# Kernel tuning notes

Hardware: AMD Instinct MI355X
Metric: run time of the kernel (lower is better)

## Reference

```python
import jax, jax.numpy as jnp
import numpy as np

N_UPDATE = 3

def _lin(key, fan_in, fan_out):
    s = 1.0 / np.sqrt(fan_in)
    k1, k2 = jax.random.split(key)
    W = jax.random.uniform(k1, (fan_in, fan_out), jnp.float32, -s, s)
    b = jax.random.uniform(k2, (fan_out,), jnp.float32, -s, s)
    return W, b

def setup_inputs() -> dict:
    key = jax.random.key(0)
    ks = jax.random.split(key, 12)
    N, E, F_NODE, F_EDGE, H, L, R, T = 50000, 400000, 16, 16, 32, 64, 128, 1
    inp = {}
    inp["x"] = jax.random.normal(ks[0], (N, F_NODE), jnp.float32)
    inp["edge_index"] = jax.random.randint(ks[1], (E, 2), 0, N)  # [E,2] (src,dst)
    inp["edge_attr"] = jax.random.normal(ks[2], (E, F_EDGE), jnp.float32)
    # edge MLP: F_EDGE -> 64 -> 64 -> H*H
    inp["Wm0"], inp["bm0"] = _lin(ks[3], F_EDGE, L)
    inp["Wm1"], inp["bm1"] = _lin(ks[4], L, L)
    inp["Wm2"], inp["bm2"] = _lin(ks[5], L, H * H)
    # NNConv root weight + bias
    inp["root"], inp["bias"] = _lin(ks[6], H, H)
    # readout i-net: 2H -> R -> T ; j-net: H -> R -> T
    inp["Wi0"], inp["bi0"] = _lin(ks[7], 2 * H, R)
    inp["Wi1"], inp["bi1"] = _lin(ks[8], R, T)
    inp["Wj0"], inp["bj0"] = _lin(ks[9], H, R)
    inp["Wj1"], inp["bj1"] = _lin(ks[10], R, T)
    return inp

def reference(x, edge_index, edge_attr, Wm0, bm0, Wm1, bm1, Wm2, bm2,
              root, bias, Wi0, bi0, Wi1, bi1, Wj0, bj0, Wj1, bj1):
    N = x.shape[0]
    H = root.shape[0]
    # h_0 = [x, zeros] padded to hidden_state_size
    h0 = jnp.concatenate([x, jnp.zeros((N, H - x.shape[1]), x.dtype)], axis=1)
    # edge MLP -> per-edge weight matrices (edge_attr constant across updates)
    e = jax.nn.relu(edge_attr @ Wm0 + bm0)
    e = jax.nn.relu(e @ Wm1 + bm1)
    W = (e @ Wm2 + bm2).reshape(-1, H, H)  # [E, H, H]
    src = edge_index[:, 0]
    dst = edge_index[:, 1]
    h = h0
    for _ in range(N_UPDATE):
        msg = jnp.einsum('eh,eho->eo', h[src], W)              # gather + bmm
        agg = jax.ops.segment_sum(msg, dst, num_segments=N)    # scatter-add
        h = h @ root + bias + agg                              # NNConv root/bias
    # mpnn readout: sum_v sigmoid(i([h_T, h_0])) * j(h_T)
    gate = jax.nn.sigmoid(jax.nn.relu(jnp.concatenate([h, h0], 1) @ Wi0 + bi0) @ Wi1 + bi1)
    val = jax.nn.relu(h @ Wj0 + bj0) @ Wj1 + bj1
    return jnp.sum(gate * val, axis=0)  # [target_size]
```

## Files before the change

### kernel.cpp

```cpp
#include <hip/hip_runtime.h>
#include <stdint.h>

#define N_UPDATE 3
#define HD 32
#define FN 16

typedef unsigned short u16;
typedef __bf16 bf16x8 __attribute__((ext_vector_type(8)));
typedef float f32x4 __attribute__((ext_vector_type(4)));

__device__ __forceinline__ float bf2f(u16 u) {
  union { uint32_t i; float f; } v; v.i = ((uint32_t)u) << 16; return v.f;
}
__device__ __forceinline__ u16 f2bf(float f) {
  union { uint32_t i; float f; } v; v.f = f;
  uint32_t x = v.i;
  return (u16)((x + 0x7fffu + ((x >> 16) & 1u)) >> 16);
}

union frag16 { uint4 v; bf16x8 b; u16 s[8]; };

__global__ void k_zero_f(float* __restrict__ p, int n) {
  int i = blockIdx.x * blockDim.x + threadIdx.x;
  if (i < n) p[i] = 0.f;
}
__global__ void k_zero_i(int* __restrict__ p, int n) {
  int i = blockIdx.x * blockDim.x + threadIdx.x;
  if (i < n) p[i] = 0;
}

__global__ void k_hist(const int* __restrict__ eidx, int* __restrict__ cnt, int E) {
  int e = blockIdx.x * blockDim.x + threadIdx.x;
  if (e >= E) return;
  atomicAdd(&cnt[eidx[2 * e]], 1);
}

__global__ __launch_bounds__(1024) void k_scan(const int* __restrict__ cnt,
                                               int* __restrict__ ptr, int N) {
  __shared__ int sums[1024];
  int chunk = (N + 1023) / 1024;
  int beg = threadIdx.x * chunk;
  int end = beg + chunk; if (end > N) end = N;
  int s = 0;
  for (int i = beg; i < end; i++) s += cnt[i];
  sums[threadIdx.x] = s;
  __syncthreads();
  for (int off = 1; off < 1024; off <<= 1) {
    int v = (threadIdx.x >= off) ? sums[threadIdx.x - off] : 0;
    __syncthreads();
    sums[threadIdx.x] += v;
    __syncthreads();
  }
  int run = (threadIdx.x == 0) ? 0 : sums[threadIdx.x - 1];
  for (int i = beg; i < end; i++) { ptr[i] = run; run += cnt[i]; }
}

__global__ void k_scatter(const int* __restrict__ eidx, int* __restrict__ ptr,
                          int* __restrict__ se_src, int* __restrict__ se_dst,
                          int* __restrict__ invp, int E) {
  int e = blockIdx.x * blockDim.x + threadIdx.x;
  if (e >= E) return;
  int2 sd = ((const int2*)eidx)[e];
  int pos = atomicAdd(&ptr[sd.x], 1);
  se_src[pos] = sd.x;
  se_dst[pos] = sd.y;
  invp[e] = pos;
}

__global__ void k_prep_bf(const float* __restrict__ Wm2, uint4* __restrict__ Bf) {
  int t = blockIdx.x;
  int lane = threadIdx.x;
  int col = lane & 15;
  int hg = lane >> 4;
  int p = t >> 6;
  int t2 = t & 63;
  int j2 = t2 * 16 + col;
  int o = p * 16 + (j2 >> 6);
  int k = j2 & 63;
  frag16 f;
#pragma unroll
  for (int jj = 0; jj < 8; jj++) {
    int h = hg * 8 + jj;
    f.s[jj] = f2bf(Wm2[k * 1024 + h * 32 + o]);
  }
  Bf[t * 64 + lane] = f.v;
}

__global__ void k_init_h(const float* __restrict__ x, float* __restrict__ h, int N) {
  int idx = blockIdx.x * blockDim.x + threadIdx.x;
  if (idx >= N * HD) return;
  int n = idx >> 5, c = idx & 31;
  h[idx] = (c < FN) ? x[n * FN + c] : 0.f;
}

__global__ __launch_bounds__(256) void k_edge_mlp(
    const float* __restrict__ ea,
    const float* __restrict__ Wm0, const float* __restrict__ bm0,
    const float* __restrict__ Wm1, const float* __restrict__ bm1,
    const int* __restrict__ invp, u16* __restrict__ ee, int E) {
  int e = blockIdx.x * blockDim.x + threadIdx.x;
  if (e >= E) return;
  float a[16];
  {
    const float4* p = (const float4*)(ea + (size_t)e * 16);
    float4 v0 = p[0], v1 = p[1], v2 = p[2], v3 = p[3];
    a[0]=v0.x; a[1]=v0.y; a[2]=v0.z; a[3]=v0.w;
    a[4]=v1.x; a[5]=v1.y; a[6]=v1.z; a[7]=v1.w;
    a[8]=v2.x; a[9]=v2.y; a[10]=v2.z; a[11]=v2.w;
    a[12]=v3.x; a[13]=v3.y; a[14]=v3.z; a[15]=v3.w;
  }
  float t0[64];
#pragma unroll
  for (int j = 0; j < 64; j++) t0[j] = bm0[j];
#pragma unroll
  for (int k = 0; k < 16; k++) {
    float av = a[k];
#pragma unroll
    for (int j = 0; j < 64; j++) t0[j] = fmaf(av, Wm0[k * 64 + j], t0[j]);
  }
#pragma unroll
  for (int j = 0; j < 64; j++) t0[j] = fmaxf(t0[j], 0.f);

  u16* dst = ee + (size_t)invp[e] * 64;
#pragma unroll
  for (int half = 0; half < 2; half++) {
    float t1[32];
#pragma unroll
    for (int j = 0; j < 32; j++) t1[j] = bm1[half * 32 + j];
#pragma unroll
    for (int k = 0; k < 64; k++) {
      float tv = t0[k];
#pragma unroll
      for (int j = 0; j < 32; j++) t1[j] = fmaf(tv, Wm1[k * 64 + half * 32 + j], t1[j]);
    }
    unsigned int out[16];
#pragma unroll
    for (int j = 0; j < 16; j++) {
      u16 lo = f2bf(fmaxf(t1[2 * j], 0.f));
      u16 hi = f2bf(fmaxf(t1[2 * j + 1], 0.f));
      out[j] = (unsigned int)lo | ((unsigned int)hi << 16);
    }
    uint4* op = (uint4*)(dst + half * 32);
#pragma unroll
    for (int q = 0; q < 4; q++) {
      uint4 w; w.x = out[q*4+0]; w.y = out[q*4+1]; w.z = out[q*4+2]; w.w = out[q*4+3];
      op[q] = w;
    }
  }
}

__global__ __launch_bounds__(256) void k_gemm_G(
    const float* __restrict__ h, const uint4* __restrict__ Bf,
    u16* __restrict__ Gb, int N, int p) {
  int wave = threadIdx.x >> 6;
  int lane = threadIdx.x & 63;
  int jt = blockIdx.y * 4 + wave;
  int n0 = blockIdx.x * 16;
  int row = lane & 15;
  int kg = lane >> 4;

  int nr = n0 + row; if (nr > N - 1) nr = N - 1;
  const float* hr = h + (size_t)nr * HD + kg * 8;
  float4 f0 = *(const float4*)hr;
  float4 f1 = *(const float4*)(hr + 4);
  frag16 a;
  a.s[0] = f2bf(f0.x); a.s[1] = f2bf(f0.y); a.s[2] = f2bf(f0.z); a.s[3] = f2bf(f0.w);
  a.s[4] = f2bf(f1.x); a.s[5] = f2bf(f1.y); a.s[6] = f2bf(f1.z); a.s[7] = f2bf(f1.w);

  frag16 b; b.v = Bf[(p * 64 + jt) * 64 + lane];

  f32x4 acc = {0.f, 0.f, 0.f, 0.f};
  acc = __builtin_amdgcn_mfma_f32_16x16x32_bf16(a.b, b.b, acc, 0, 0, 0);

  int j2 = jt * 16 + row;
#pragma unroll
  for (int r = 0; r < 4; r++) {
    int n = n0 + kg * 4 + r;
    if (n < N) Gb[(size_t)n * 1024 + j2] = f2bf(acc[r]);
  }
}

__global__ __launch_bounds__(256) void k_msg(
    const u16* __restrict__ Gb, const float* __restrict__ h,
    const float* __restrict__ bm2, const u16* __restrict__ ee,
    const int* __restrict__ se_src, const int* __restrict__ se_dst,
    float* __restrict__ agg, int E, int p) {
  int t = blockIdx.x * blockDim.x + threadIdx.x;
  int e = t >> 4;
  int o_l = t & 15;
  if (e >= E) return;
  int src = se_src[e];
  int dst = se_dst[e];
  int o = p * 16 + o_l;

  float hv0 = h[(size_t)src * HD + o_l];
  float hv1 = h[(size_t)src * HD + 16 + o_l];
  float acc = 0.f;
#pragma unroll
  for (int hh = 0; hh < 16; hh++) {
    acc = fmaf(__shfl(hv0, hh, 16), bm2[hh * 32 + o], acc);
    acc = fmaf(__shfl(hv1, hh, 16), bm2[(hh + 16) * 32 + o], acc);
  }

  const uint4* ep = (const uint4*)(ee + (size_t)e * 64);
  const uint4* gp = (const uint4*)(Gb + ((size_t)src * 16 + o_l) * 64);
  frag16 eu[8], gu[8];
#pragma unroll
  for (int q = 0; q < 8; q++) { eu[q].v = ep[q]; gu[q].v = gp[q]; }
#pragma unroll
  for (int k = 0; k < 64; k++) {
    acc = fmaf(bf2f(eu[k >> 3].s[k & 7]), bf2f(gu[k >> 3].s[k & 7]), acc);
  }
  atomicAdd(&agg[(size_t)dst * HD + o], acc);
}

__global__ __launch_bounds__(256) void k_update(
    const float* __restrict__ h, float* __restrict__ agg,
    const float* __restrict__ root, const float* __restrict__ bias,
    float* __restrict__ hn, int N) {
  int t = blockIdx.x * blockDim.x + threadIdx.x;
  int n = t >> 5, o = t & 31;
  if (n >= N) return;
  float hv = h[(size_t)n * HD + o];
  float acc = bias[o] + agg[(size_t)n * HD + o];
  agg[(size_t)n * HD + o] = 0.f;
#pragma unroll
  for (int k = 0; k < 32; k++)
    acc = fmaf(__shfl(hv, k, 32), root[k * HD + o], acc);
  hn[(size_t)n * HD + o] = acc;
}

__global__ __launch_bounds__(256) void k_readout(
    const float* __restrict__ h, const float* __restrict__ x,
    const float* __restrict__ Wi0, const float* __restrict__ bi0,
    const float* __restrict__ Wi1, const float* __restrict__ bi1,
    const float* __restrict__ Wj0, const float* __restrict__ bj0,
    const float* __restrict__ Wj1, const float* __restrict__ bj1,
    float* __restrict__ partial, int N) {
  int wid = threadIdx.x >> 6;
  int lane = threadIdx.x & 63;
  int n = blockIdx.x * 4 + wid;
  __shared__ float sred[4];
  float contrib = 0.f;
  if (n < N) {
    float uv;
    if (lane < 32) uv = h[(size_t)n * HD + lane];
    else if (lane < 48) uv = x[(size_t)n * FN + lane - 32];
    else uv = 0.f;

    float g1a = bi0[lane], g1b = bi0[lane + 64];
#pragma unroll
    for (int k = 0; k < 64; k++) {
      float u = __shfl(uv, k, 64);
      g1a = fmaf(u, Wi0[k * 128 + lane], g1a);
      g1b = fmaf(u, Wi0[k * 128 + lane + 64], g1b);
    }
    g1a = fmaxf(g1a, 0.f); g1b = fmaxf(g1b, 0.f);
    float gp = g1a * Wi1[lane] + g1b * Wi1[lane + 64];

    float v1a = bj0[lane], v1b = bj0[lane + 64];
#pragma unroll
    for (int k = 0; k < 32; k++) {
      float hk = __shfl(uv, k, 64);
      v1a = fmaf(hk, Wj0[k * 128 + lane], v1a);
      v1b = fmaf(hk, Wj0[k * 128 + lane + 64], v1b);
    }
    v1a = fmaxf(v1a, 0.f); v1b = fmaxf(v1b, 0.f);
    float vp = v1a * Wj1[lane] + v1b * Wj1[lane + 64];

#pragma unroll
    for (int s = 32; s; s >>= 1) {
      gp += __shfl_xor(gp, s, 64);
      vp += __shfl_xor(vp, s, 64);
    }
    float gate = 1.f / (1.f + __expf(-(gp + bi1[0])));
    float val = vp + bj1[0];
    contrib = gate * val;
  }
  if (lane == 0) sred[wid] = contrib;
  __syncthreads();
  if (threadIdx.x == 0) partial[blockIdx.x] = sred[0] + sred[1] + sred[2] + sred[3];
}

__global__ void k_final(const float* __restrict__ partial, float* __restrict__ out, int P) {
  __shared__ float sm[256];
  float s = 0.f;
  for (int i = threadIdx.x; i < P; i += 256) s += partial[i];
  sm[threadIdx.x] = s;
  __syncthreads();
  for (int st = 128; st; st >>= 1) {
    if ((int)threadIdx.x < st) sm[threadIdx.x] += sm[threadIdx.x + st];
    __syncthreads();
  }
  if (threadIdx.x == 0) out[0] = sm[0];
}

extern "C" void kernel_launch(void* const* d_in, const int* in_sizes, int n_in,
                              void* d_out, int out_size, void* d_ws, size_t ws_size,
                              hipStream_t stream) {
  const float* x    = (const float*)d_in[0];
  const int*   eidx = (const int*)d_in[1];
  const float* ea   = (const float*)d_in[2];
  const float* Wm0  = (const float*)d_in[3];
  const float* bm0  = (const float*)d_in[4];
  const float* Wm1  = (const float*)d_in[5];
  const float* bm1  = (const float*)d_in[6];
  const float* Wm2  = (const float*)d_in[7];
  const float* bm2  = (const float*)d_in[8];
  const float* root = (const float*)d_in[9];
  const float* bias = (const float*)d_in[10];
  const float* Wi0  = (const float*)d_in[11];
  const float* bi0  = (const float*)d_in[12];
  const float* Wi1  = (const float*)d_in[13];
  const float* bi1  = (const float*)d_in[14];
  const float* Wj0  = (const float*)d_in[15];
  const float* bj0  = (const float*)d_in[16];
  const float* Wj1  = (const float*)d_in[17];
  const float* bj1  = (const float*)d_in[18];

  int N = in_sizes[0] / FN;
  int E = in_sizes[1] / 2;
  int nb = (N + 3) / 4;

  auto al = [](size_t b) { return (b + 255) & ~(size_t)255; };
  size_t need = al((size_t)N * 1024 * 2) + al((size_t)E * 64 * 2) +
                al(128 * 64 * sizeof(uint4)) + 3 * al((size_t)N * HD * 4) +
                2 * al((size_t)N * 4) + 3 * al((size_t)E * 4) + al((size_t)nb * 4);
  if (need > ws_size) return;

  char* ws = (char*)d_ws;
  size_t off = 0;
  auto alloc = [&](size_t bytes) { void* p = ws + off; off += al(bytes); return p; };
  u16*   Gb      = (u16*)alloc((size_t)N * 1024 * 2);
  u16*   ee      = (u16*)alloc((size_t)E * 64 * 2);
  uint4* Bf      = (uint4*)alloc(128 * 64 * sizeof(uint4));
  float* hA      = (float*)alloc((size_t)N * HD * 4);
  float* hB      = (float*)alloc((size_t)N * HD * 4);
  float* agg     = (float*)alloc((size_t)N * HD * 4);
  int*   cnt     = (int*)alloc((size_t)N * 4);
  int*   ptr     = (int*)alloc((size_t)N * 4);
  int*   se_src  = (int*)alloc((size_t)E * 4);
  int*   se_dst  = (int*)alloc((size_t)E * 4);
  int*   invp    = (int*)alloc((size_t)E * 4);
  float* partial = (float*)alloc((size_t)nb * 4);

  int mt = (N + 15) / 16;
  int ng = (N * HD + 255) / 256;
  int eg = (E + 255) / 256;

  hipLaunchKernelGGL(k_zero_i, dim3((N + 255) / 256), dim3(256), 0, stream, cnt, N);
  hipLaunchKernelGGL(k_hist, dim3(eg), dim3(256), 0, stream, eidx, cnt, E);
  hipLaunchKernelGGL(k_scan, dim3(1), dim3(1024), 0, stream, cnt, ptr, N);
  hipLaunchKernelGGL(k_scatter, dim3(eg), dim3(256), 0, stream, eidx, ptr, se_src, se_dst, invp, E);

  hipLaunchKernelGGL(k_prep_bf, dim3(128), dim3(64), 0, stream, Wm2, Bf);
  hipLaunchKernelGGL(k_init_h, dim3(ng), dim3(256), 0, stream, x, hA, N);
  hipLaunchKernelGGL(k_edge_mlp, dim3(eg), dim3(256), 0, stream,
                     ea, Wm0, bm0, Wm1, bm1, invp, ee, E);
  hipLaunchKernelGGL(k_zero_f, dim3(ng), dim3(256), 0, stream, agg, N * HD);

  float* hc = hA; float* hn = hB;
  for (int it = 0; it < N_UPDATE; it++) {
    for (int p = 0; p < 2; p++) {
      hipLaunchKernelGGL(k_gemm_G, dim3(mt, 16), dim3(256), 0, stream, hc, Bf, Gb, N, p);
      hipLaunchKernelGGL(k_msg, dim3(((size_t)E * 16 + 255) / 256), dim3(256), 0, stream,
                         Gb, hc, bm2, ee, se_src, se_dst, agg, E, p);
    }
    hipLaunchKernelGGL(k_update, dim3(ng), dim3(256), 0, stream,
                       hc, agg, root, bias, hn, N);
    float* tmp = hc; hc = hn; hn = tmp;
  }

  hipLaunchKernelGGL(k_readout, dim3(nb), dim3(256), 0, stream,
                     hc, x, Wi0, bi0, Wi1, bi1, Wj0, bj0, Wj1, bj1, partial, N);
  hipLaunchKernelGGL(k_final, dim3(1), dim3(256), 0, stream, partial, (float*)d_out, nb);
}
```

Baseline: 1.607 ms.

## Replace atomic scatter-add with dst-sorted message buffer and CSR gather aggregation

Messages are no longer atomically added into agg. Each edge writes its message to a slot grouped by destination, and a fused aggregate-update kernel sums each node's incoming slots through a destination CSR before applying root and bias. The per-node h·bm2 bias term is also precomputed once per node in the update kernel and init kernel, so edges no longer recompute it. This removes float atomics and the agg zeroing, at the cost of an E×32 float message buffer, extra preprocessing (a second histogram, a second scan and dstpos), and scattered writes and reads.

Result: slower. 1.686 ms (+4.9%).

```diff
diff --git a/kernel.cpp b/kernel.cpp
--- a/kernel.cpp
+++ b/kernel.cpp
@@ -20,27 +20,28 @@
 
 union frag16 { uint4 v; bf16x8 b; u16 s[8]; };
 
-__global__ void k_zero_f(float* __restrict__ p, int n) {
-  int i = blockIdx.x * blockDim.x + threadIdx.x;
-  if (i < n) p[i] = 0.f;
-}
 __global__ void k_zero_i(int* __restrict__ p, int n) {
   int i = blockIdx.x * blockDim.x + threadIdx.x;
   if (i < n) p[i] = 0;
 }
 
-__global__ void k_hist(const int* __restrict__ eidx, int* __restrict__ cnt, int E) {
+__global__ void k_hist2(const int* __restrict__ eidx, int* __restrict__ cntS,
+                        int* __restrict__ cntD, int E) {
   int e = blockIdx.x * blockDim.x + threadIdx.x;
   if (e >= E) return;
-  atomicAdd(&cnt[eidx[2 * e]], 1);
+  int2 sd = ((const int2*)eidx)[e];
+  atomicAdd(&cntS[sd.x], 1);
+  atomicAdd(&cntD[sd.y], 1);
 }
 
 __global__ __launch_bounds__(1024) void k_scan(const int* __restrict__ cnt,
-                                               int* __restrict__ ptr, int N) {
+                                               int* __restrict__ out1,
+                                               int* __restrict__ out2, int N) {
   __shared__ int sums[1024];
   int chunk = (N + 1023) / 1024;
   int beg = threadIdx.x * chunk;
   int end = beg + chunk; if (end > N) end = N;
+  if (beg > N) beg = N;
   int s = 0;
   for (int i = beg; i < end; i++) s += cnt[i];
   sums[threadIdx.x] = s;
@@ -52,19 +53,34 @@
     __syncthreads();
   }
   int run = (threadIdx.x == 0) ? 0 : sums[threadIdx.x - 1];
-  for (int i = beg; i < end; i++) { ptr[i] = run; run += cnt[i]; }
-}
-
-__global__ void k_scatter(const int* __restrict__ eidx, int* __restrict__ ptr,
-                          int* __restrict__ se_src, int* __restrict__ se_dst,
-                          int* __restrict__ invp, int E) {
+  for (int i = beg; i < end; i++) {
+    out1[i] = run;
+    if (out2) out2[i] = run;
+    run += cnt[i];
+  }
+  if (end == N) {
+    out1[N] = run;
+    if (out2) out2[N] = run;
+  }
+}
+
+__global__ void k_scatter_src(const int* __restrict__ eidx, int* __restrict__ ptrS,
+                              int* __restrict__ se_src, int* __restrict__ se_dst,
+                              int* __restrict__ invp, int E) {
   int e = blockIdx.x * blockDim.x + threadIdx.x;
   if (e >= E) return;
   int2 sd = ((const int2*)eidx)[e];
-  int pos = atomicAdd(&ptr[sd.x], 1);
+  int pos = atomicAdd(&ptrS[sd.x], 1);
   se_src[pos] = sd.x;
   se_dst[pos] = sd.y;
   invp[e] = pos;
+}
+
+__global__ void k_dstpos(const int* __restrict__ se_dst, int* __restrict__ ptrD,
+                         int* __restrict__ dstpos, int E) {
+  int q = blockIdx.x * blockDim.x + threadIdx.x;
+  if (q >= E) return;
+  dstpos[q] = atomicAdd(&ptrD[se_dst[q]], 1);
 }
 
 __global__ void k_prep_bf(const float* __restrict__ Wm2, uint4* __restrict__ Bf) {
@@ -86,11 +102,18 @@
   Bf[t * 64 + lane] = f.v;
 }
 
-__global__ void k_init_h(const float* __restrict__ x, float* __restrict__ h, int N) {
+__global__ void k_init_h(const float* __restrict__ x, const float* __restrict__ bm2,
+                         float* __restrict__ h, float* __restrict__ hbbuf, int N) {
   int idx = blockIdx.x * blockDim.x + threadIdx.x;
   if (idx >= N * HD) return;
-  int n = idx >> 5, c = idx & 31;
-  h[idx] = (c < FN) ? x[n * FN + c] : 0.f;
+  int n = idx >> 5, o = idx & 31;
+  float v = (o < FN) ? x[n * FN + o] : 0.f;
+  h[idx] = v;
+  float hb = 0.f;
+#pragma unroll
+  for (int k = 0; k < 32; k++)
+    hb = fmaf(__shfl(v, k, 32), bm2[k * 32 + o], hb);
+  hbbuf[idx] = hb;
 }
 
 __global__ __launch_bounds__(256) void k_edge_mlp(
@@ -181,26 +204,16 @@
 }
 
 __global__ __launch_bounds__(256) void k_msg(
-    const u16* __restrict__ Gb, const float* __restrict__ h,
-    const float* __restrict__ bm2, const u16* __restrict__ ee,
-    const int* __restrict__ se_src, const int* __restrict__ se_dst,
-    float* __restrict__ agg, int E, int p) {
+    const u16* __restrict__ Gb, const float* __restrict__ hbbuf,
+    const u16* __restrict__ ee, const int* __restrict__ se_src,
+    const int* __restrict__ dstpos, float* __restrict__ msgbuf, int E, int p) {
   int t = blockIdx.x * blockDim.x + threadIdx.x;
   int e = t >> 4;
   int o_l = t & 15;
   if (e >= E) return;
   int src = se_src[e];
-  int dst = se_dst[e];
-  int o = p * 16 + o_l;
-
-  float hv0 = h[(size_t)src * HD + o_l];
-  float hv1 = h[(size_t)src * HD + 16 + o_l];
-  float acc = 0.f;
-#pragma unroll
-  for (int hh = 0; hh < 16; hh++) {
-    acc = fmaf(__shfl(hv0, hh, 16), bm2[hh * 32 + o], acc);
-    acc = fmaf(__shfl(hv1, hh, 16), bm2[(hh + 16) * 32 + o], acc);
-  }
+
+  float acc = hbbuf[(size_t)src * HD + p * 16 + o_l];
 
   const uint4* ep = (const uint4*)(ee + (size_t)e * 64);
   const uint4* gp = (const uint4*)(Gb + ((size_t)src * 16 + o_l) * 64);
@@ -211,23 +224,33 @@
   for (int k = 0; k < 64; k++) {
     acc = fmaf(bf2f(eu[k >> 3].s[k & 7]), bf2f(gu[k >> 3].s[k & 7]), acc);
   }
-  atomicAdd(&agg[(size_t)dst * HD + o], acc);
-}
-
-__global__ __launch_bounds__(256) void k_update(
-    const float* __restrict__ h, float* __restrict__ agg,
-    const float* __restrict__ root, const float* __restrict__ bias,
-    float* __restrict__ hn, int N) {
+  msgbuf[(size_t)dstpos[e] * HD + p * 16 + o_l] = acc;
+}
+
+__global__ __launch_bounds__(256) void k_aggupd(
+    const float* __restrict__ msgbuf, const int* __restrict__ rowptrD,
+    const float* __restrict__ h, const float* __restrict__ root,
+    const float* __restrict__ bias, const float* __restrict__ bm2,
+    float* __restrict__ hn, float* __restrict__ hbbuf, int N) {
   int t = blockIdx.x * blockDim.x + threadIdx.x;
   int n = t >> 5, o = t & 31;
   if (n >= N) return;
+  int jb = rowptrD[n], je = rowptrD[n + 1];
+  float s = 0.f;
+  for (int j = jb; j < je; j++) s += msgbuf[(size_t)j * HD + o];
+
   float hv = h[(size_t)n * HD + o];
-  float acc = bias[o] + agg[(size_t)n * HD + o];
-  agg[(size_t)n * HD + o] = 0.f;
+  float acc = bias[o] + s;
 #pragma unroll
   for (int k = 0; k < 32; k++)
     acc = fmaf(__shfl(hv, k, 32), root[k * HD + o], acc);
   hn[(size_t)n * HD + o] = acc;
+
+  float hb = 0.f;
+#pragma unroll
+  for (int k = 0; k < 32; k++)
+    hb = fmaf(__shfl(acc, k, 32), bm2[k * 32 + o], hb);
+  hbbuf[(size_t)n * HD + o] = hb;
 }
 
 __global__ __launch_bounds__(256) void k_readout(
@@ -323,9 +346,15 @@
   int nb = (N + 3) / 4;
 
   auto al = [](size_t b) { return (b + 255) & ~(size_t)255; };
-  size_t need = al((size_t)N * 1024 * 2) + al((size_t)E * 64 * 2) +
-                al(128 * 64 * sizeof(uint4)) + 3 * al((size_t)N * HD * 4) +
-                2 * al((size_t)N * 4) + 3 * al((size_t)E * 4) + al((size_t)nb * 4);
+  size_t need = al((size_t)N * 1024 * 2)
+              + al((size_t)E * 64 * 2)
+              + al((size_t)E * HD * 4)
+              + al(128 * 64 * sizeof(uint4))
+              + 3 * al((size_t)N * HD * 4)
+              + 2 * al((size_t)N * 4)
+              + 3 * al(((size_t)N + 1) * 4)
+              + 4 * al((size_t)E * 4)
+              + al((size_t)nb * 4);
   if (need > ws_size) return;
 
   char* ws = (char*)d_ws;
@@ -333,41 +362,49 @@
   auto alloc = [&](size_t bytes) { void* p = ws + off; off += al(bytes); return p; };
   u16*   Gb      = (u16*)alloc((size_t)N * 1024 * 2);
   u16*   ee      = (u16*)alloc((size_t)E * 64 * 2);
+  float* msgbuf  = (float*)alloc((size_t)E * HD * 4);
   uint4* Bf      = (uint4*)alloc(128 * 64 * sizeof(uint4));
   float* hA      = (float*)alloc((size_t)N * HD * 4);
   float* hB      = (float*)alloc((size_t)N * HD * 4);
-  float* agg     = (float*)alloc((size_t)N * HD * 4);
-  int*   cnt     = (int*)alloc((size_t)N * 4);
-  int*   ptr     = (int*)alloc((size_t)N * 4);
+  float* hbbuf   = (float*)alloc((size_t)N * HD * 4);
+  int*   cntS    = (int*)alloc((size_t)N * 4);
+  int*   cntD    = (int*)alloc((size_t)N * 4);
+  int*   ptrS    = (int*)alloc(((size_t)N + 1) * 4);
+  int*   rowptrD = (int*)alloc(((size_t)N + 1) * 4);
+  int*   ptrD    = (int*)alloc(((size_t)N + 1) * 4);
   int*   se_src  = (int*)alloc((size_t)E * 4);
   int*   se_dst  = (int*)alloc((size_t)E * 4);
   int*   invp    = (int*)alloc((size_t)E * 4);
+  int*   dstpos  = (int*)alloc((size_t)E * 4);
   float* partial = (float*)alloc((size_t)nb * 4);
 
   int mt = (N + 15) / 16;
   int ng = (N * HD + 255) / 256;
   int eg = (E + 255) / 256;
 
-  hipLaunchKernelGGL(k_zero_i, dim3((N + 255) / 256), dim3(256), 0, stream, cnt, N);
-  hipLaunchKernelGGL(k_hist, dim3(eg), dim3(256), 0, stream, eidx, cnt, E);
-  hipLaunchKernelGGL(k_scan, dim3(1), dim3(1024), 0, stream, cnt, ptr, N);
-  hipLaunchKernelGGL(k_scatter, dim3(eg), dim3(256), 0, stream, eidx, ptr, se_src, se_dst, invp, E);
+  int zn = (int)(((char*)cntD - (char*)cntS) / 4) + N;
+  hipLaunchKernelGGL(k_zero_i, dim3((zn + 255) / 256), dim3(256), 0, stream, cntS, zn);
+  hipLaunchKernelGGL(k_hist2, dim3(eg), dim3(256), 0, stream, eidx, cntS, cntD, E);
+  hipLaunchKernelGGL(k_scan, dim3(1), dim3(1024), 0, stream, cntS, ptrS, (int*)nullptr, N);
+  hipLaunchKernelGGL(k_scan, dim3(1), dim3(1024), 0, stream, cntD, rowptrD, ptrD, N);
+  hipLaunchKernelGGL(k_scatter_src, dim3(eg), dim3(256), 0, stream,
+                     eidx, ptrS, se_src, se_dst, invp, E);
+  hipLaunchKernelGGL(k_dstpos, dim3(eg), dim3(256), 0, stream, se_dst, ptrD, dstpos, E);
 
   hipLaunchKernelGGL(k_prep_bf, dim3(128), dim3(64), 0, stream, Wm2, Bf);
-  hipLaunchKernelGGL(k_init_h, dim3(ng), dim3(256), 0, stream, x, hA, N);
+  hipLaunchKernelGGL(k_init_h, dim3(ng), dim3(256), 0, stream, x, bm2, hA, hbbuf, N);
   hipLaunchKernelGGL(k_edge_mlp, dim3(eg), dim3(256), 0, stream,
                      ea, Wm0, bm0, Wm1, bm1, invp, ee, E);
-  hipLaunchKernelGGL(k_zero_f, dim3(ng), dim3(256), 0, stream, agg, N * HD);
 
   float* hc = hA; float* hn = hB;
   for (int it = 0; it < N_UPDATE; it++) {
     for (int p = 0; p < 2; p++) {
       hipLaunchKernelGGL(k_gemm_G, dim3(mt, 16), dim3(256), 0, stream, hc, Bf, Gb, N, p);
       hipLaunchKernelGGL(k_msg, dim3(((size_t)E * 16 + 255) / 256), dim3(256), 0, stream,
-                         Gb, hc, bm2, ee, se_src, se_dst, agg, E, p);
-    }
-    hipLaunchKernelGGL(k_update, dim3(ng), dim3(256), 0, stream,
-                       hc, agg, root, bias, hn, N);
+                         Gb, hbbuf, ee, se_src, dstpos, msgbuf, E, p);
+    }
+    hipLaunchKernelGGL(k_aggupd, dim3(ng), dim3(256), 0, stream,
+                       msgbuf, rowptrD, hc, root, bias, bm2, hn, hbbuf, N);
     float* tmp = hc; hc = hn; hn = tmp;
   }
 
```
